# Performance work log

Hardware: AMD Instinct MI355X
Metric: run time of the kernel (lower is better)

## Reference

```python
import jax, jax.numpy as jnp
import numpy as np

K = 16      # n_sample neighbors
L = 2       # stacked PT blocks
D = 128     # in_dim
H = 128     # hidden_dim = out_dim = vector_dim
EPS = 1e-5


def _bn(x, g, b, axes):
    # batch-norm with batch statistics (train-mode MinkowskiBatchNorm / BN1d / BN2d)
    m = jnp.mean(x, axes, keepdims=True)
    v = jnp.var(x, axes, keepdims=True)
    return (x - m) * jax.lax.rsqrt(v + EPS) * g + b


def setup_inputs():
    key = jax.random.key(0)
    ks = jax.random.split(key, 16)
    B, Nper = 2, 8192
    coords = jax.random.randint(ks[0], (B, Nper, 3), 0, 200, dtype=jnp.int32)
    feats = jax.random.normal(ks[1], (B * Nper, D), dtype=jnp.float32)
    w = lambda k, s: jax.random.normal(k, s, dtype=jnp.float32) * 0.1
    return {
        'coords': coords, 'feats': feats,
        'W_top': w(ks[2], (L, D, H)),
        'bn_top_g': jnp.ones((L, H)), 'bn_top_b': jnp.zeros((L, H)),
        'W_phi': w(ks[3], (L, H, H)),
        'W_psi': w(ks[4], (L, H, H)),
        'W_alpha': w(ks[5], (L, H, H)),
        'W_d1': w(ks[6], (L, 3, H)), 'b_d1': jnp.zeros((L, H)),
        'bn_d1_g': jnp.ones((L, H)), 'bn_d1_b': jnp.zeros((L, H)),
        'W_d2': w(ks[7], (L, H, H)), 'b_d2': jnp.zeros((L, H)),
        'bn_d2_g': jnp.ones((L, H)), 'bn_d2_b': jnp.zeros((L, H)),
        'W_g1': w(ks[8], (L, H, H)), 'b_g1': jnp.zeros((L, H)),
        'bn_g1_g': jnp.ones((L, H)), 'bn_g1_b': jnp.zeros((L, H)),
        'W_g2': w(ks[9], (L, H, H)), 'b_g2': jnp.zeros((L, H)),
        'bn_g2_g': jnp.ones((L, H)), 'bn_g2_b': jnp.zeros((L, H)),
        'W_down': w(ks[10], (L, H, D)),
        'bn_down_g': jnp.ones((L, D)), 'bn_down_b': jnp.zeros((L, D)),
    }


def _knn(coords):
    # cube_query with USE_KNN=True: per-scene KNN grouping (self included)
    cf = coords.astype(jnp.float32)

    def one(c):  # c: (Nper, 3)
        d2 = jnp.sum((c[:, None, :] - c[None, :, :]) ** 2, -1)  # (Nper, Nper)
        _, idx = jax.lax.top_k(-d2, K)
        return idx

    idx = jax.vmap(one)(cf)                      # (B, Nper, K) per-scene indices
    nbr = jax.vmap(lambda c, i: c[i])(cf, idx)   # (B, Nper, K, 3) grouped coords
    rel = nbr - cf[:, :, None, :]                # relative xyz (pose input)
    B, Nper = coords.shape[0], coords.shape[1]
    gidx = (idx + (jnp.arange(B, dtype=idx.dtype) * Nper)[:, None, None]).reshape(-1, K)
    return rel.reshape(-1, K, 3), gidx           # (N,K,3), (N,K) global indices


def reference(coords, feats, W_top, bn_top_g, bn_top_b, W_phi, W_psi, W_alpha,
              W_d1, b_d1, bn_d1_g, bn_d1_b, W_d2, b_d2, bn_d2_g, bn_d2_b,
              W_g1, b_g1, bn_g1_g, bn_g1_b, W_g2, b_g2, bn_g2_g, bn_g2_b,
              W_down, bn_down_g, bn_down_b):
    rel, gidx = _knn(coords)
    f = feats
    for l in range(L):
        h = _bn(f @ W_top[l], bn_top_g[l], bn_top_b[l], 0)  # linear_top (1x1 conv + BN)
        # delta: pointwise MLP 3 -> H -> H on relative xyz (position encoding)
        pose = jax.nn.relu(_bn(rel @ W_d1[l] + b_d1[l], bn_d1_g[l], bn_d1_b[l], (0, 1)))
        pose = _bn(pose @ W_d2[l] + b_d2[l], bn_d2_g[l], bn_d2_b[l], (0, 1))  # (N,K,H)
        q = h @ W_phi[l]               # (N, H)
        kk = (h @ W_psi[l])[gidx]      # neighbor keys   (N, K, H)
        v = (h @ W_alpha[l])[gidx]     # neighbor values (N, K, H)
        # gamma: pointwise MLP on (phi - psi + pose), vector attention logits
        a = q[:, None, :] - kk + pose
        a = jax.nn.relu(_bn(a @ W_g1[l] + b_g1[l], bn_g1_g[l], bn_g1_b[l], (0, 1)))
        a = _bn(a @ W_g2[l] + b_g2[l], bn_g2_g[l], bn_g2_b[l], (0, 1))
        attn = jax.nn.softmax(a, axis=1)          # per-channel softmax over K neighbors
        y = jnp.sum(attn * (v + pose), axis=1)    # (N, H) vector-attention aggregation
        y = _bn(y @ W_down[l], bn_down_g[l], bn_down_b[l], 0)  # linear_down + BN
        f = y + f                                  # residual
    return f
```

## Files before the change

### kernel.cpp

```cpp
#include <hip/hip_runtime.h>

using u16 = unsigned short;
using u32 = unsigned int;
using u64 = unsigned long long;

#define NPTS   16384
#define NPER   8192
#define KNN    16
#define NKROWS (NPTS*KNN)
#define HD     128
#define CAP    208
#define NSLOT  16

typedef _Float16 half8 __attribute__((ext_vector_type(8)));
typedef float    floatx4 __attribute__((ext_vector_type(4)));

__device__ __forceinline__ u16  f2h(float f){ _Float16 h=(_Float16)f; return __builtin_bit_cast(u16,h); }
__device__ __forceinline__ float h2f(u16 u){ return (float)__builtin_bit_cast(_Float16,u); }
__device__ __forceinline__ u32 umin32(u32 a,u32 b){ return a<b?a:b; }

__global__ __launch_bounds__(256) void pack_coords(const int* __restrict__ coords, u32* __restrict__ pc){
    int i = blockIdx.x*256 + threadIdx.x;
    pc[i] = (u32)coords[3*i] | ((u32)coords[3*i+1]<<8) | ((u32)coords[3*i+2]<<16);
}

struct WPtrs { const float* p[8]; };
__global__ __launch_bounds__(256) void prep_weights(WPtrs wp, u16* __restrict__ wt){
    int idx = blockIdx.x*256 + threadIdx.x;
    int t = idx>>15, rem = idx&32767;
    int l = rem>>14, e = rem&16383;
    int n = e>>7, k = e&127;
    wt[idx] = f2h(wp.p[t][l*16384 + k*128 + n]);
}

__global__ __launch_bounds__(512) void knn3(const u32* __restrict__ pc, int* __restrict__ idx_g,
                                            float* __restrict__ rel, u64* __restrict__ sM){
    __shared__ u32 sc[NPER];
    __shared__ u32 buf[8][CAP];
    __shared__ u64 red[9];
    int tid = threadIdx.x;
    int wave = tid>>6, lane = tid&63;
    int scene = blockIdx.x >> 10;
    int q = (blockIdx.x & 1023)*8 + wave;

    const uint4* s4 = (const uint4*)(pc + scene*NPER);
#pragma unroll
    for (int i=0;i<4;i++) ((uint4*)sc)[tid + i*512] = s4[tid + i*512];
    if (tid<9) red[tid]=0;
    if (lane<16) buf[wave][lane]=0xFFFFFFFFu;
    __syncthreads();

    u32 qp = sc[q];
    int qx=(int)(qp&255), qy=(int)((qp>>8)&255), qz=(int)((qp>>16)&255);
    u32 thresh = 0xFFFFFFFFu;
    u32 cnt = 16;

    auto merge = [&](){
        u32 v0 = (lane      < (int)cnt) ? buf[wave][lane]      : 0xFFFFFFFFu;
        u32 v1 = (lane+64   < (int)cnt) ? buf[wave][lane+64]   : 0xFFFFFFFFu;
        u32 v2 = (lane+128  < (int)cnt) ? buf[wave][lane+128]  : 0xFFFFFFFFu;
        u32 v3 = (lane+192  < (int)cnt) ? buf[wave][lane+192]  : 0xFFFFFFFFu;
        u32 out = 0;
#pragma unroll
        for (int r=0;r<16;r++){
            u32 m = umin32(umin32(v0,v1),umin32(v2,v3));
#pragma unroll
            for (int o=32;o>=1;o>>=1) m = umin32(m, (u32)__shfl_xor((int)m, o, 64));
            if      (v0==m) v0=0xFFFFFFFFu;
            else if (v1==m) v1=0xFFFFFFFFu;
            else if (v2==m) v2=0xFFFFFFFFu;
            else if (v3==m) v3=0xFFFFFFFFu;
            if (lane==r) out = m;
            thresh = m;
        }
        if (lane<16) buf[wave][lane] = out;
        cnt = 16;
    };

    int lane2 = lane*2;
    uint2 p2 = ((const uint2*)sc)[lane];
    for (int t=0;t<64;t++){
        uint2 cur = p2;
        if (t<63) p2 = ((const uint2*)sc)[(t+1)*64+lane];
        int base = t*128 + lane2;
        u32 pa = cur.x;
        int dx0=(int)(pa&255)-qx, dy0=(int)((pa>>8)&255)-qy, dz0=(int)((pa>>16)&255)-qz;
        u32 d2_0 = (u32)(__mul24(dx0,dx0)+__mul24(dy0,dy0)+__mul24(dz0,dz0));
        u32 key0 = (d2_0<<13) + (u32)base;
        u32 pb = cur.y;
        int dx1=(int)(pb&255)-qx, dy1=(int)((pb>>8)&255)-qy, dz1=(int)((pb>>16)&255)-qz;
        u32 d2_1 = (u32)(__mul24(dx1,dx1)+__mul24(dy1,dy1)+__mul24(dz1,dz1));
        u32 key1 = (d2_1<<13) + (u32)(base+1);
        u64 m0 = __ballot(key0 < thresh);
        if (m0){
            u32 lt = __builtin_amdgcn_mbcnt_hi((u32)(m0>>32), __builtin_amdgcn_mbcnt_lo((u32)m0,0));
            if (key0 < thresh) buf[wave][cnt + lt] = key0;
            cnt += (u32)__popcll(m0);
        }
        u64 m1 = __ballot(key1 < thresh);
        if (m1){
            u32 lt = __builtin_amdgcn_mbcnt_hi((u32)(m1>>32), __builtin_amdgcn_mbcnt_lo((u32)m1,0));
            if (key1 < thresh) buf[wave][cnt + lt] = key1;
            cnt += (u32)__popcll(m1);
        }
        if (cnt > CAP-128) merge();
    }
    merge();

    int n = scene*NPER + q;
    u32 key = buf[wave][lane & 15];
    int dx=0,dy=0,dz=0;
    if (lane<16){
        int j = (int)(key & 8191u);
        idx_g[(size_t)n*KNN + lane] = scene*NPER + j;
        u32 p = sc[j];
        dx=(int)(p&255)-qx; dy=(int)((p>>8)&255)-qy; dz=(int)((p>>16)&255)-qz;
        size_t ro = ((size_t)n*KNN+lane)*3;
        rel[ro]=(float)dx; rel[ro+1]=(float)dy; rel[ro+2]=(float)dz;
    }
    int arr[9] = {dx,dy,dz, dx*dx,dy*dy,dz*dz, dx*dy,dx*dz,dy*dz};
#pragma unroll
    for (int o=32;o>=1;o>>=1)
#pragma unroll
        for (int j=0;j<9;j++) arr[j] += __shfl_xor(arr[j], o, 64);
    if (lane==0)
#pragma unroll
        for (int j=0;j<9;j++) atomicAdd(&red[j], (u64)(long long)arr[j]);
    __syncthreads();
    if (tid<9) atomicAdd(&sM[tid], red[tid]);
}

__global__ __launch_bounds__(256) void finalize_d1(const u64* __restrict__ sM, const float* __restrict__ W_d1,
        const float* __restrict__ b_d1, const float* __restrict__ g, const float* __restrict__ beta,
        float* __restrict__ A, float* __restrict__ C){
    int tid=threadIdx.x; int l=tid>>7, c=tid&127;
    double s0=(double)(long long)sM[0], s1=(double)(long long)sM[1], s2=(double)(long long)sM[2];
    double m00=(double)(long long)sM[3], m11=(double)(long long)sM[4], m22=(double)(long long)sM[5];
    double m01=(double)(long long)sM[6], m02=(double)(long long)sM[7], m12=(double)(long long)sM[8];
    double w0=W_d1[l*384+c], w1=W_d1[l*384+128+c], w2=W_d1[l*384+256+c];
    double b =b_d1[l*128+c];
    double S = s0*w0+s1*w1+s2*w2;
    double Q = m00*w0*w0+m11*w1*w1+m22*w2*w2 + 2.0*(m01*w0*w1+m02*w0*w2+m12*w1*w2);
    double cnt = (double)NKROWS;
    double mean = S/cnt + b;
    double ex2  = (Q + 2.0*b*S)/cnt + b*b;
    double var  = ex2 - mean*mean;
    float a = g[l*128+c] * (float)(1.0/sqrt(var+1e-5));
    A[l*128+c]=a; C[l*128+c]=beta[l*128+c]-(float)mean*a;
}

__global__ void finalize_affine(double* __restrict__ P, const float* __restrict__ g,
        const float* __restrict__ b, double cnt, float* __restrict__ A, float* __restrict__ C){
    int c=threadIdx.x;
    double s=0.0, q=0.0;
#pragma unroll
    for (int k=0;k<NSLOT;k++){
        s+=P[k*256+c]; q+=P[k*256+128+c];
        P[k*256+c]=0.0; P[k*256+128+c]=0.0;
    }
    double mean=s/cnt, var=q/cnt-mean*mean;
    float a = g[c] * (float)(1.0/sqrt(var+1e-5));
    A[c]=a; C[c]=b[c]-(float)mean*a;
}

struct CompF32 {
    const float* src;
    __device__ __forceinline__ void stage(u16* As,int R0,int k0,int tid) const {
#pragma unroll
        for (int u=0;u<8;u++){
            int flat=u*256+tid, row=flat>>4, c4=flat&15; int k=k0+c4*4;
            const float4 v=*(const float4*)(src+(size_t)(R0+row)*HD+k);
            ushort4 o; o.x=f2h(v.x); o.y=f2h(v.y); o.z=f2h(v.z); o.w=f2h(v.w);
            *(ushort4*)(As+row*72+c4*4)=o;
        }
    }
};
struct CompH16Aff {
    const u16* src; const float* Aa; const float* Ca;
    __device__ __forceinline__ void stage(u16* As,int R0,int k0,int tid) const {
#pragma unroll
        for (int u=0;u<8;u++){
            int flat=u*256+tid, row=flat>>4, c4=flat&15; int k=k0+c4*4;
            const ushort4 v=*(const ushort4*)(src+(size_t)(R0+row)*HD+k);
            ushort4 o;
            o.x=f2h(h2f(v.x)*Aa[k]  +Ca[k]);   o.y=f2h(h2f(v.y)*Aa[k+1]+Ca[k+1]);
            o.z=f2h(h2f(v.z)*Aa[k+2]+Ca[k+2]); o.w=f2h(h2f(v.w)*Aa[k+3]+Ca[k+3]);
            *(ushort4*)(As+row*72+c4*4)=o;
        }
    }
};
struct CompH16AffRelu {
    const u16* src; const float* Aa; const float* Ca;
    __device__ __forceinline__ void stage(u16* As,int R0,int k0,int tid) const {
#pragma unroll
        for (int u=0;u<8;u++){
            int flat=u*256+tid, row=flat>>4, c4=flat&15; int k=k0+c4*4;
            const ushort4 v=*(const ushort4*)(src+(size_t)(R0+row)*HD+k);
            ushort4 o;
            o.x=f2h(fmaxf(h2f(v.x)*Aa[k]  +Ca[k],  0.f));
            o.y=f2h(fmaxf(h2f(v.y)*Aa[k+1]+Ca[k+1],0.f));
            o.z=f2h(fmaxf(h2f(v.z)*Aa[k+2]+Ca[k+2],0.f));
            o.w=f2h(fmaxf(h2f(v.w)*Aa[k+3]+Ca[k+3],0.f));
            *(ushort4*)(As+row*72+c4*4)=o;
        }
    }
};
struct CompPose1 {
    const float* rel; const float* Wd1; const float* bd1; const float* Aa; const float* Ca;
    __device__ __forceinline__ void stage(u16* As,int R0,int k0,int tid) const {
#pragma unroll
        for (int u=0;u<8;u++){
            int flat=u*256+tid, row=flat>>4, c4=flat&15; int k=k0+c4*4; int R=R0+row;
            float r0=rel[(size_t)R*3], r1=rel[(size_t)R*3+1], r2=rel[(size_t)R*3+2];
            ushort4 o;
#pragma unroll
            for (int j=0;j<4;j++){
                int kk=k+j;
                float x = r0*Wd1[kk] + r1*Wd1[HD+kk] + r2*Wd1[2*HD+kk] + bd1[kk];
                x = fmaxf(x*Aa[kk]+Ca[kk], 0.f);
                ((u16*)&o)[j]=f2h(x);
            }
            *(ushort4*)(As+row*72+c4*4)=o;
        }
    }
};
struct CompA0 {
    const u16* q; const u16* kp; const u16* pose; const int* gidx; const float* Aa; const float* Ca;
    __device__ __forceinline__ void stage(u16* As,int R0,int k0,int tid) const {
#pragma unroll
        for (int u=0;u<8;u++){
            int flat=u*256+tid, row=flat>>4, c4=flat&15; int k=k0+c4*4; int R=R0+row;
            int n=R>>4; int g=gidx[R];
            const ushort4 qv=*(const ushort4*)(q +(size_t)n*HD+k);
            const ushort4 kv=*(const ushort4*)(kp+(size_t)g*HD+k);
            const ushort4 pv=*(const ushort4*)(pose+(size_t)R*HD+k);
            ushort4 o;
            o.x=f2h(h2f(qv.x)-h2f(kv.x) + h2f(pv.x)*Aa[k]  +Ca[k]);
            o.y=f2h(h2f(qv.y)-h2f(kv.y) + h2f(pv.y)*Aa[k+1]+Ca[k+1]);
            o.z=f2h(h2f(qv.z)-h2f(kv.z) + h2f(pv.z)*Aa[k+2]+Ca[k+2]);
            o.w=f2h(h2f(qv.w)-h2f(kv.w) + h2f(pv.w)*Aa[k+3]+Ca[k+3]);
            *(ushort4*)(As+row*72+c4*4)=o;
        }
    }
};

template<class Comp, bool OUT16, bool HASBIAS, bool STATS>
__global__ __launch_bounds__(256) void gemm128(Comp comp, const u16* __restrict__ Wt,
        const float* __restrict__ bias, void* __restrict__ outp, double* __restrict__ statsP,
        int wtStride, long outStride){
    __shared__ __align__(16) u16 As[128*72];
    __shared__ __align__(16) u16 Bs[128*72];
    __shared__ float cs2[2][128], cq2[2][128];
    const u16* W = Wt + (size_t)blockIdx.y*wtStride;
    u16*   o16 = (u16*)outp   + (size_t)blockIdx.y*outStride;
    float* o32 = (float*)outp + (size_t)blockIdx.y*outStride;
    int tid=threadIdx.x;
    int R0=blockIdx.x*128;
    int lane=tid&63, wave=tid>>6, quad=lane>>4, r16=lane&15;
    int wm=wave>>1, wn=wave&1;
    floatx4 acc[4][4]={};
#pragma unroll
    for (int ks=0;ks<2;ks++){
        int k0=ks*64;
        comp.stage(As,R0,k0,tid);
#pragma unroll
        for (int u=0;u<4;u++){
            int flat=u*256+tid, n=flat>>3, c8=flat&7;
            *(int4*)(Bs+n*72+c8*8) = *(const int4*)(W+n*HD+k0+c8*8);
        }
        __syncthreads();
#pragma unroll
        for (int kk2=0;kk2<2;kk2++){
            half8 aF[4], bF[4];
#pragma unroll
            for (int mi=0;mi<4;mi++) aF[mi]=*(const half8*)(As+(wm*64+mi*16+r16)*72 + kk2*32+quad*8);
#pragma unroll
            for (int ni=0;ni<4;ni++) bF[ni]=*(const half8*)(Bs+(wn*64+ni*16+r16)*72 + kk2*32+quad*8);
#pragma unroll
            for (int mi=0;mi<4;mi++)
#pragma unroll
                for (int ni=0;ni<4;ni++)
                    acc[mi][ni]=__builtin_amdgcn_mfma_f32_16x16x32_f16(aF[mi],bF[ni],acc[mi][ni],0,0,0);
        }
        __syncthreads();
    }
    float sAcc[4]={0,0,0,0}, qAcc[4]={0,0,0,0};
#pragma unroll
    for (int mi=0;mi<4;mi++)
#pragma unroll
        for (int ni=0;ni<4;ni++){
            int col=wn*64+ni*16+r16;
            float bv = HASBIAS ? bias[col] : 0.f;
#pragma unroll
            for (int rg=0;rg<4;rg++){
                int row=R0+wm*64+mi*16+quad*4+rg;
                float v=acc[mi][ni][rg]+bv;
                if (STATS){ sAcc[ni]+=v; qAcc[ni]+=v*v; }
                if (OUT16) o16[(size_t)row*HD+col]=f2h(v);
                else       o32[(size_t)row*HD+col]=v;
            }
        }
    if (STATS){
#pragma unroll
        for (int ni=0;ni<4;ni++){
            float s=sAcc[ni], q=qAcc[ni];
            s += __shfl_xor(s,16,64); s += __shfl_xor(s,32,64);
            q += __shfl_xor(q,16,64); q += __shfl_xor(q,32,64);
            if (quad==0){
                int col=wn*64+ni*16+r16;
                cs2[wm][col]=s; cq2[wm][col]=q;
            }
        }
        __syncthreads();
        if (tid<128){
            int slot = blockIdx.x & (NSLOT-1);
            unsafeAtomicAdd(&statsP[slot*256+tid],     (double)(cs2[0][tid]+cs2[1][tid]));
            unsafeAtomicAdd(&statsP[slot*256+128+tid], (double)(cq2[0][tid]+cq2[1][tid]));
        }
    }
}

__global__ __launch_bounds__(256) void aggregate(const u16* __restrict__ a2, const u16* __restrict__ pose,
        const u16* __restrict__ vv, const int* __restrict__ gidx,
        const float* __restrict__ Ag2, const float* __restrict__ Cg2,
        const float* __restrict__ Ad2, const float* __restrict__ Cd2, float* __restrict__ y){
    int c=(threadIdx.x&63)*2, h=threadIdx.x>>6;
    int n=blockIdx.x*4+h;
    float sA0=Ag2[c], sC0=Cg2[c], pA0=Ad2[c], pC0=Cd2[c];
    float sA1=Ag2[c+1], sC1=Cg2[c+1], pA1=Ad2[c+1], pC1=Cd2[c+1];
    float av0[16], av1[16]; float m0=-1e30f, m1=-1e30f;
#pragma unroll
    for (int k=0;k<16;k++){
        ushort2 t=*(const ushort2*)(a2+((size_t)n*16+k)*HD+c);
        float a0=h2f(t.x)*sA0+sC0, a1=h2f(t.y)*sA1+sC1;
        av0[k]=a0; av1[k]=a1; m0=fmaxf(m0,a0); m1=fmaxf(m1,a1);
    }
    float sum0=0.f, sum1=0.f;
#pragma unroll
    for (int k=0;k<16;k++){
        float e0=__expf(av0[k]-m0), e1=__expf(av1[k]-m1);
        av0[k]=e0; av1[k]=e1; sum0+=e0; sum1+=e1;
    }
    float acc0=0.f, acc1=0.f;
#pragma unroll
    for (int k=0;k<16;k++){
        int g=gidx[n*16+k];
        ushort2 pt=*(const ushort2*)(pose+((size_t)n*16+k)*HD+c);
        ushort2 vt=*(const ushort2*)(vv+(size_t)g*HD+c);
        acc0 += av0[k]*(h2f(pt.x)*pA0+pC0 + h2f(vt.x));
        acc1 += av1[k]*(h2f(pt.y)*pA1+pC1 + h2f(vt.y));
    }
    y[(size_t)n*HD+c]  =acc0/sum0;
    y[(size_t)n*HD+c+1]=acc1/sum1;
}

__global__ __launch_bounds__(256) void residual(const float* __restrict__ ydown, const float* __restrict__ A,
        const float* __restrict__ C, const float* __restrict__ fin, float* __restrict__ fout){
    size_t i=(size_t)blockIdx.x*256+threadIdx.x; int c=(int)(i&127);
    fout[i]=ydown[i]*A[c]+C[c]+fin[i];
}

extern "C" void kernel_launch(void* const* d_in, const int* in_sizes, int n_in,
                              void* d_out, int out_size, void* d_ws, size_t ws_size,
                              hipStream_t stream){
    const int*   coords=(const int*)d_in[0];
    const float* feats=(const float*)d_in[1];
    const float* W_top=(const float*)d_in[2];
    const float* g_top=(const float*)d_in[3];
    const float* bt_top=(const float*)d_in[4];
    const float* W_phi=(const float*)d_in[5];
    const float* W_psi=(const float*)d_in[6];
    const float* W_alp=(const float*)d_in[7];
    const float* W_d1=(const float*)d_in[8];
    const float* b_d1=(const float*)d_in[9];
    const float* g_d1=(const float*)d_in[10];
    const float* bt_d1=(const float*)d_in[11];
    const float* W_d2=(const float*)d_in[12];
    const float* b_d2=(const float*)d_in[13];
    const float* g_d2=(const float*)d_in[14];
    const float* bt_d2=(const float*)d_in[15];
    const float* W_g1=(const float*)d_in[16];
    const float* b_g1=(const float*)d_in[17];
    const float* g_g1=(const float*)d_in[18];
    const float* bt_g1=(const float*)d_in[19];
    const float* W_g2=(const float*)d_in[20];
    const float* b_g2=(const float*)d_in[21];
    const float* g_g2=(const float*)d_in[22];
    const float* bt_g2=(const float*)d_in[23];
    const float* W_dn=(const float*)d_in[24];
    const float* g_dn=(const float*)d_in[25];
    const float* bt_dn=(const float*)d_in[26];

    char* ws=(char*)d_ws;
    size_t off=0;
    auto carve=[&](size_t bytes)->char*{ char* p=ws+off; off=(off+bytes+255)&~(size_t)255; return p; };
    u32*    pc    =(u32*)   carve((size_t)NPTS*4);
    int*    idxg  =(int*)   carve((size_t)NKROWS*4);
    float*  rel   =(float*) carve((size_t)NKROWS*3*4);
    u16*    h16   =(u16*)   carve((size_t)NPTS*HD*2);
    u16*    qb    =(u16*)   carve((size_t)3*NPTS*HD*2);
    u16*    kpb   = qb + (size_t)NPTS*HD;
    u16*    vvb   = qb + (size_t)2*NPTS*HD;
    float*  yb    =(float*) carve((size_t)NPTS*HD*4);
    float*  ydown =(float*) carve((size_t)NPTS*HD*4);
    float*  fbuf  =(float*) carve((size_t)NPTS*HD*4);
    u16*    wt    =(u16*)   carve((size_t)8*2*16384*2);
    char*   stats =         carve(NSLOT*256*8 + 256);
    double* P     =(double*)stats;
    u64*    sM    =(u64*)(stats + NSLOT*256*8);
    float*  aff   =(float*) carve(8192);
    float *A_top=aff, *C_top=aff+128, *A_d2=aff+256, *C_d2=aff+384,
          *A_g1=aff+512, *C_g1=aff+640, *A_g2=aff+768, *C_g2=aff+896,
          *A_dn=aff+1024, *C_dn=aff+1152, *A_d1=aff+1280, *C_d1=aff+1536;
    u16*    pose2 =(u16*)   carve((size_t)NKROWS*HD*2);
    u16*    abuf  =(u16*)   carve((size_t)NKROWS*HD*2);
    if (ws_size < off) return;

    hipMemsetAsync(stats, 0, NSLOT*256*8 + 256, stream);
    pack_coords<<<dim3(NPTS/256),dim3(256),0,stream>>>(coords, pc);
    WPtrs wp{{W_top,W_phi,W_psi,W_alp,W_d2,W_g1,W_g2,W_dn}};
    prep_weights<<<dim3(8*2*16384/256),dim3(256),0,stream>>>(wp, wt);
    knn3<<<dim3(2048),dim3(512),0,stream>>>(pc, idxg, rel, sM);
    finalize_d1<<<dim3(1),dim3(256),0,stream>>>(sM, W_d1, b_d1, g_d1, bt_d1, A_d1, C_d1);

    const float* fin=feats;
    for (int l=0;l<2;l++){
        const u16* wt_top=wt+(0*2+l)*16384; const u16* wt_phi=wt+(1*2+l)*16384;
        const u16* wt_d2 =wt+(4*2+l)*16384; const u16* wt_g1 =wt+(5*2+l)*16384;
        const u16* wt_g2 =wt+(6*2+l)*16384; const u16* wt_dn =wt+(7*2+l)*16384;

        gemm128<CompF32,true,false,true><<<dim3(NPTS/128),dim3(256),0,stream>>>(
            CompF32{fin}, wt_top, nullptr, h16, P, 0, 0);
        finalize_affine<<<dim3(1),dim3(128),0,stream>>>(P, g_top+l*128, bt_top+l*128, (double)NPTS, A_top, C_top);

        gemm128<CompH16Aff,true,false,false><<<dim3(NPTS/128,3),dim3(256),0,stream>>>(
            CompH16Aff{h16,A_top,C_top}, wt_phi, nullptr, qb, nullptr, 2*16384, (long)NPTS*HD);

        gemm128<CompPose1,true,true,true><<<dim3(NKROWS/128),dim3(256),0,stream>>>(
            CompPose1{rel, W_d1+l*384, b_d1+l*128, A_d1+l*128, C_d1+l*128}, wt_d2, b_d2+l*128, pose2, P, 0, 0);
        finalize_affine<<<dim3(1),dim3(128),0,stream>>>(P, g_d2+l*128, bt_d2+l*128, (double)NKROWS, A_d2, C_d2);

        gemm128<CompA0,true,true,true><<<dim3(NKROWS/128),dim3(256),0,stream>>>(
            CompA0{qb,kpb,pose2,idxg,A_d2,C_d2}, wt_g1, b_g1+l*128, abuf, P, 0, 0);
        finalize_affine<<<dim3(1),dim3(128),0,stream>>>(P, g_g1+l*128, bt_g1+l*128, (double)NKROWS, A_g1, C_g1);

        gemm128<CompH16AffRelu,true,true,true><<<dim3(NKROWS/128),dim3(256),0,stream>>>(
            CompH16AffRelu{abuf,A_g1,C_g1}, wt_g2, b_g2+l*128, abuf, P, 0, 0);
        finalize_affine<<<dim3(1),dim3(128),0,stream>>>(P, g_g2+l*128, bt_g2+l*128, (double)NKROWS, A_g2, C_g2);

        aggregate<<<dim3(NPTS/4),dim3(256),0,stream>>>(abuf, pose2, vvb, idxg, A_g2, C_g2, A_d2, C_d2, yb);

        gemm128<CompF32,false,false,true><<<dim3(NPTS/128),dim3(256),0,stream>>>(
            CompF32{yb}, wt_dn, nullptr, ydown, P, 0, 0);
        finalize_affine<<<dim3(1),dim3(128),0,stream>>>(P, g_dn+l*128, bt_dn+l*128, (double)NPTS, A_dn, C_dn);
        residual<<<dim3(NPTS*HD/256),dim3(256),0,stream>>>(ydown, A_dn, C_dn, fin, (l==1)?(float*)d_out:fbuf);
        fin=fbuf;
    }
}
```

Baseline: 559.5 us.

## Use uniform-grid KNN and fold pose/query-key paths into the gamma-1 GEMM

Result: slower. 705.1 us (+26.0%).

```diff
diff --git a/kernel.cpp b/kernel.cpp
--- a/kernel.cpp
+++ b/kernel.cpp
@@ -9,7 +9,7 @@
 #define KNN    16
 #define NKROWS (NPTS*KNN)
 #define HD     128
-#define CAP    208
+#define KCAP   512
 #define NSLOT  16
 
 typedef _Float16 half8 __attribute__((ext_vector_type(8)));
@@ -18,94 +18,136 @@
 __device__ __forceinline__ u16  f2h(float f){ _Float16 h=(_Float16)f; return __builtin_bit_cast(u16,h); }
 __device__ __forceinline__ float h2f(u16 u){ return (float)__builtin_bit_cast(_Float16,u); }
 __device__ __forceinline__ u32 umin32(u32 a,u32 b){ return a<b?a:b; }
-
-__global__ __launch_bounds__(256) void pack_coords(const int* __restrict__ coords, u32* __restrict__ pc){
+__device__ __forceinline__ int cell_of(int x){ return (x*5243)>>17; }
+
+__global__ __launch_bounds__(256) void pack_count(const int* __restrict__ coords, u32* __restrict__ pc,
+                                                  u32* __restrict__ cellcnt){
     int i = blockIdx.x*256 + threadIdx.x;
-    pc[i] = (u32)coords[3*i] | ((u32)coords[3*i+1]<<8) | ((u32)coords[3*i+2]<<16);
-}
-
-struct WPtrs { const float* p[8]; };
-__global__ __launch_bounds__(256) void prep_weights(WPtrs wp, u16* __restrict__ wt){
-    int idx = blockIdx.x*256 + threadIdx.x;
-    int t = idx>>15, rem = idx&32767;
-    int l = rem>>14, e = rem&16383;
-    int n = e>>7, k = e&127;
-    wt[idx] = f2h(wp.p[t][l*16384 + k*128 + n]);
-}
-
-__global__ __launch_bounds__(512) void knn3(const u32* __restrict__ pc, int* __restrict__ idx_g,
-                                            float* __restrict__ rel, u64* __restrict__ sM){
-    __shared__ u32 sc[NPER];
-    __shared__ u32 buf[8][CAP];
+    int x=coords[3*i], y=coords[3*i+1], z=coords[3*i+2];
+    pc[i] = (u32)x | ((u32)y<<8) | ((u32)z<<16);
+    int cid = ((cell_of(z)*8 + cell_of(y))<<3) + cell_of(x);
+    atomicAdd(&cellcnt[(i>>13)*512 + cid], 1u);
+}
+
+__global__ __launch_bounds__(1024) void prefix1024(const u32* __restrict__ cellcnt,
+                                                   u32* __restrict__ cs, u32* __restrict__ cptr){
+    __shared__ u32 tmp[1024];
+    int t = threadIdx.x;
+    u32 mine = cellcnt[t];
+    tmp[t] = mine;
+    __syncthreads();
+    for (int off=1; off<1024; off<<=1){
+        u32 v = (t>=off) ? tmp[t-off] : 0u;
+        __syncthreads();
+        tmp[t] += v;
+        __syncthreads();
+    }
+    if (t==0) cs[0]=0;
+    cs[t+1] = tmp[t];
+    cptr[t] = tmp[t] - mine;
+}
+
+__global__ __launch_bounds__(256) void scatter_pts(const u32* __restrict__ pc, u32* __restrict__ cptr,
+                                                   uint2* __restrict__ spt){
+    int i = blockIdx.x*256 + threadIdx.x;
+    u32 p = pc[i];
+    int cid = ((cell_of((int)((p>>16)&255))*8 + cell_of((int)((p>>8)&255)))<<3) + cell_of((int)(p&255));
+    u32 pos = atomicAdd(&cptr[(i>>13)*512 + cid], 1u);
+    spt[pos] = make_uint2(p, (u32)(i&8191));
+}
+
+__global__ __launch_bounds__(256) void knn_grid(const u32* __restrict__ pc, const uint2* __restrict__ spt,
+                                                const u32* __restrict__ cs, int* __restrict__ idx_g,
+                                                float* __restrict__ rel, u64* __restrict__ sM){
+    __shared__ u32 buf[4][KCAP];
     __shared__ u64 red[9];
     int tid = threadIdx.x;
     int wave = tid>>6, lane = tid&63;
-    int scene = blockIdx.x >> 10;
-    int q = (blockIdx.x & 1023)*8 + wave;
-
-    const uint4* s4 = (const uint4*)(pc + scene*NPER);
-#pragma unroll
-    for (int i=0;i<4;i++) ((uint4*)sc)[tid + i*512] = s4[tid + i*512];
+    int scene = blockIdx.x >> 11;
+    int q = (blockIdx.x & 2047)*4 + wave;
     if (tid<9) red[tid]=0;
     if (lane<16) buf[wave][lane]=0xFFFFFFFFu;
     __syncthreads();
 
-    u32 qp = sc[q];
+    u32 qp = pc[scene*NPER + q];
     int qx=(int)(qp&255), qy=(int)((qp>>8)&255), qz=(int)((qp>>16)&255);
+    int cx=cell_of(qx), cy=cell_of(qy), cz=cell_of(qz);
     u32 thresh = 0xFFFFFFFFu;
     u32 cnt = 16;
 
     auto merge = [&](){
-        u32 v0 = (lane      < (int)cnt) ? buf[wave][lane]      : 0xFFFFFFFFu;
-        u32 v1 = (lane+64   < (int)cnt) ? buf[wave][lane+64]   : 0xFFFFFFFFu;
-        u32 v2 = (lane+128  < (int)cnt) ? buf[wave][lane+128]  : 0xFFFFFFFFu;
-        u32 v3 = (lane+192  < (int)cnt) ? buf[wave][lane+192]  : 0xFFFFFFFFu;
+        u32 v[8];
+#pragma unroll
+        for (int r=0;r<8;r++) v[r] = ((u32)(lane + r*64) < cnt) ? buf[wave][lane + r*64] : 0xFFFFFFFFu;
         u32 out = 0;
 #pragma unroll
-        for (int r=0;r<16;r++){
-            u32 m = umin32(umin32(v0,v1),umin32(v2,v3));
+        for (int it=0; it<16; it++){
+            u32 m = umin32(umin32(umin32(v[0],v[1]),umin32(v[2],v[3])),
+                           umin32(umin32(v[4],v[5]),umin32(v[6],v[7])));
 #pragma unroll
             for (int o=32;o>=1;o>>=1) m = umin32(m, (u32)__shfl_xor((int)m, o, 64));
-            if      (v0==m) v0=0xFFFFFFFFu;
-            else if (v1==m) v1=0xFFFFFFFFu;
-            else if (v2==m) v2=0xFFFFFFFFu;
-            else if (v3==m) v3=0xFFFFFFFFu;
-            if (lane==r) out = m;
+#pragma unroll
+            for (int r=0;r<8;r++) if (v[r]==m) v[r]=0xFFFFFFFFu;
+            if (lane==it) out = m;
             thresh = m;
         }
         if (lane<16) buf[wave][lane] = out;
         cnt = 16;
     };
 
-    int lane2 = lane*2;
-    uint2 p2 = ((const uint2*)sc)[lane];
-    for (int t=0;t<64;t++){
-        uint2 cur = p2;
-        if (t<63) p2 = ((const uint2*)sc)[(t+1)*64+lane];
-        int base = t*128 + lane2;
-        u32 pa = cur.x;
-        int dx0=(int)(pa&255)-qx, dy0=(int)((pa>>8)&255)-qy, dz0=(int)((pa>>16)&255)-qz;
-        u32 d2_0 = (u32)(__mul24(dx0,dx0)+__mul24(dy0,dy0)+__mul24(dz0,dz0));
-        u32 key0 = (d2_0<<13) + (u32)base;
-        u32 pb = cur.y;
-        int dx1=(int)(pb&255)-qx, dy1=(int)((pb>>8)&255)-qy, dz1=(int)((pb>>16)&255)-qz;
-        u32 d2_1 = (u32)(__mul24(dx1,dx1)+__mul24(dy1,dy1)+__mul24(dz1,dz1));
-        u32 key1 = (d2_1<<13) + (u32)(base+1);
-        u64 m0 = __ballot(key0 < thresh);
-        if (m0){
-            u32 lt = __builtin_amdgcn_mbcnt_hi((u32)(m0>>32), __builtin_amdgcn_mbcnt_lo((u32)m0,0));
-            if (key0 < thresh) buf[wave][cnt + lt] = key0;
-            cnt += (u32)__popcll(m0);
-        }
-        u64 m1 = __ballot(key1 < thresh);
-        if (m1){
-            u32 lt = __builtin_amdgcn_mbcnt_hi((u32)(m1>>32), __builtin_amdgcn_mbcnt_lo((u32)m1,0));
-            if (key1 < thresh) buf[wave][cnt + lt] = key1;
-            cnt += (u32)__popcll(m1);
-        }
-        if (cnt > CAP-128) merge();
-    }
+    auto scan64 = [&](u32 key){
+        u64 mask = __ballot(key < thresh);
+        if (mask){
+            u32 lt = __builtin_amdgcn_mbcnt_hi((u32)(mask>>32), __builtin_amdgcn_mbcnt_lo((u32)mask,0));
+            if (key < thresh) buf[wave][cnt + lt] = key;
+            cnt += (u32)__popcll(mask);
+            if (cnt > KCAP-64) merge();
+        }
+    };
+
+    int x0 = cx>0?cx-1:0, x1 = cx<7?cx+1:7;
+    int y0 = cy>0?cy-1:0, y1 = cy<7?cy+1:7;
+    int z0 = cz>0?cz-1:0, z1 = cz<7?cz+1:7;
+    int sbase = scene*512;
+    int nx = x1-x0+1;
+    for (int rz=z0; rz<=z1; rz++)
+        for (int ry=y0; ry<=y1; ry++){
+            int c0 = sbase + ((rz*8+ry)<<3) + x0;
+            int s = (int)cs[c0], e = (int)cs[c0+nx];
+            for (int i=s; i<e; i+=64){
+                int p = i + lane;
+                u32 key = 0xFFFFFFFFu;
+                if (p < e){
+                    uint2 pt = spt[p];
+                    int dx=(int)(pt.x&255)-qx, dy=(int)((pt.x>>8)&255)-qy, dz=(int)((pt.x>>16)&255)-qz;
+                    u32 d2 = (u32)(__mul24(dx,dx)+__mul24(dy,dy)+__mul24(dz,dz));
+                    key = (d2<<13) | pt.y;
+                }
+                scan64(key);
+            }
+        }
     merge();
+
+    int d2_16 = (int)(thresh>>13);
+    int mxl = (cx==0)?1000: qx - 25*(cx-1);
+    int mxr = (cx==7)?1000: 25*(cx+2) - qx;
+    int myl = (cy==0)?1000: qy - 25*(cy-1);
+    int myr = (cy==7)?1000: 25*(cy+2) - qy;
+    int mzl = (cz==0)?1000: qz - 25*(cz-1);
+    int mzr = (cz==7)?1000: 25*(cz+2) - qz;
+    int m = min(min(min(mxl,mxr),min(myl,myr)),min(mzl,mzr));
+    if (d2_16 > m*m){
+        thresh = 0xFFFFFFFFu; cnt = 16;
+        if (lane<16) buf[wave][lane]=0xFFFFFFFFu;
+        const u32* sp = pc + scene*NPER;
+        for (int t=0;t<128;t++){
+            u32 p = sp[t*64+lane];
+            int dx=(int)(p&255)-qx, dy=(int)((p>>8)&255)-qy, dz=(int)((p>>16)&255)-qz;
+            u32 d2 = (u32)(__mul24(dx,dx)+__mul24(dy,dy)+__mul24(dz,dz));
+            scan64((d2<<13) | (u32)(t*64+lane));
+        }
+        merge();
+    }
 
     int n = scene*NPER + q;
     u32 key = buf[wave][lane & 15];
@@ -113,7 +155,7 @@
     if (lane<16){
         int j = (int)(key & 8191u);
         idx_g[(size_t)n*KNN + lane] = scene*NPER + j;
-        u32 p = sc[j];
+        u32 p = pc[scene*NPER + j];
         dx=(int)(p&255)-qx; dy=(int)((p>>8)&255)-qy; dz=(int)((p>>16)&255)-qz;
         size_t ro = ((size_t)n*KNN+lane)*3;
         rel[ro]=(float)dx; rel[ro+1]=(float)dy; rel[ro+2]=(float)dz;
@@ -128,6 +170,16 @@
         for (int j=0;j<9;j++) atomicAdd(&red[j], (u64)(long long)arr[j]);
     __syncthreads();
     if (tid<9) atomicAdd(&sM[tid], red[tid]);
+}
+
+struct WPtrs { const float* p[5]; };
+__global__ __launch_bounds__(256) void prep_weights(WPtrs wp, u16* __restrict__ wt){
+    const int tmap[5] = {0,3,4,6,7};
+    int idx = blockIdx.x*256 + threadIdx.x;
+    int t = idx>>15, rem = idx&32767;
+    int l = rem>>14, e = rem&16383;
+    int n = e>>7, k = e&127;
+    wt[(tmap[t]*2+l)*16384 + n*128 + k] = f2h(wp.p[t][l*16384 + k*128 + n]);
 }
 
 __global__ __launch_bounds__(256) void finalize_d1(const u64* __restrict__ sM, const float* __restrict__ W_d1,
@@ -150,7 +202,10 @@
 }
 
 __global__ void finalize_affine(double* __restrict__ P, const float* __restrict__ g,
-        const float* __restrict__ b, double cnt, float* __restrict__ A, float* __restrict__ C){
+        const float* __restrict__ b, double cnt, float* __restrict__ A, float* __restrict__ C,
+        const float* __restrict__ Wg1, const float* __restrict__ b_d2, const float* __restrict__ b_g1,
+        float* __restrict__ biasc){
+    __shared__ float term[128];
     int c=threadIdx.x;
     double s=0.0, q=0.0;
 #pragma unroll
@@ -160,12 +215,33 @@
     }
     double mean=s/cnt, var=q/cnt-mean*mean;
     float a = g[c] * (float)(1.0/sqrt(var+1e-5));
-    A[c]=a; C[c]=b[c]-(float)mean*a;
+    float cc = b[c]-(float)mean*a;
+    A[c]=a; C[c]=cc;
+    if (Wg1){
+        term[c] = b_d2[c]*a + cc;
+        __syncthreads();
+        float acc = b_g1[c];
+        for (int n=0;n<128;n++) acc += term[n]*Wg1[n*128+c];
+        biasc[c] = acc;
+    }
 }
 
 struct CompF32 {
     const float* src;
     __device__ __forceinline__ void stage(u16* As,int R0,int k0,int tid) const {
+#pragma unroll
+        for (int u=0;u<8;u++){
+            int flat=u*256+tid, row=flat>>4, c4=flat&15; int k=k0+c4*4;
+            const float4 v=*(const float4*)(src+(size_t)(R0+row)*HD+k);
+            ushort4 o; o.x=f2h(v.x); o.y=f2h(v.y); o.z=f2h(v.z); o.w=f2h(v.w);
+            *(ushort4*)(As+row*72+c4*4)=o;
+        }
+    }
+};
+struct CompStatic {
+    const float* p[4];
+    __device__ __forceinline__ void stage(u16* As,int R0,int k0,int tid) const {
+        const float* src = p[blockIdx.y];
 #pragma unroll
         for (int u=0;u<8;u++){
             int flat=u*256+tid, row=flat>>4, c4=flat&15; int k=k0+c4*4;
@@ -224,30 +300,14 @@
         }
     }
 };
-struct CompA0 {
-    const u16* q; const u16* kp; const u16* pose; const int* gidx; const float* Aa; const float* Ca;
-    __device__ __forceinline__ void stage(u16* As,int R0,int k0,int tid) const {
-#pragma unroll
-        for (int u=0;u<8;u++){
-            int flat=u*256+tid, row=flat>>4, c4=flat&15; int k=k0+c4*4; int R=R0+row;
-            int n=R>>4; int g=gidx[R];
-            const ushort4 qv=*(const ushort4*)(q +(size_t)n*HD+k);
-            const ushort4 kv=*(const ushort4*)(kp+(size_t)g*HD+k);
-            const ushort4 pv=*(const ushort4*)(pose+(size_t)R*HD+k);
-            ushort4 o;
-            o.x=f2h(h2f(qv.x)-h2f(kv.x) + h2f(pv.x)*Aa[k]  +Ca[k]);
-            o.y=f2h(h2f(qv.y)-h2f(kv.y) + h2f(pv.y)*Aa[k+1]+Ca[k+1]);
-            o.z=f2h(h2f(qv.z)-h2f(kv.z) + h2f(pv.z)*Aa[k+2]+Ca[k+2]);
-            o.w=f2h(h2f(qv.w)-h2f(kv.w) + h2f(pv.w)*Aa[k+3]+Ca[k+3]);
-            *(ushort4*)(As+row*72+c4*4)=o;
-        }
-    }
-};
-
-template<class Comp, bool OUT16, bool HASBIAS, bool STATS>
-__global__ __launch_bounds__(256) void gemm128(Comp comp, const u16* __restrict__ Wt,
+
+struct BTS { const float* p[4]; const float* scale; };
+
+template<class Comp, bool OUT16, bool HASBIAS, bool STATS, bool EPIQK, bool BT, bool OUTT>
+__global__ __launch_bounds__(256) void gemm128(Comp comp, const u16* __restrict__ Wt, BTS bts,
         const float* __restrict__ bias, void* __restrict__ outp, double* __restrict__ statsP,
-        int wtStride, long outStride){
+        int wtStride, long outStride,
+        const u16* __restrict__ eq, const u16* __restrict__ ek, const int* __restrict__ egidx){
     __shared__ __align__(16) u16 As[128*72];
     __shared__ __align__(16) u16 Bs[128*72];
     __shared__ float cs2[2][128], cq2[2][128];
@@ -263,10 +323,27 @@
     for (int ks=0;ks<2;ks++){
         int k0=ks*64;
         comp.stage(As,R0,k0,tid);
-#pragma unroll
-        for (int u=0;u<4;u++){
-            int flat=u*256+tid, n=flat>>3, c8=flat&7;
-            *(int4*)(Bs+n*72+c8*8) = *(const int4*)(W+n*HD+k0+c8*8);
+        if (BT){
+            const float* Bf = bts.p[blockIdx.y];
+#pragma unroll
+            for (int u=0;u<4;u++){
+                int flat=u*256+tid, n=flat>>3, c8=flat&7;
+                __align__(16) u16 tmp[8];
+#pragma unroll
+                for (int e=0;e<8;e++){
+                    int k=k0+c8*8+e;
+                    float v = Bf[(size_t)k*128+n];
+                    if (bts.scale) v *= bts.scale[k];
+                    tmp[e]=f2h(v);
+                }
+                *(int4*)(Bs+n*72+c8*8) = *(int4*)tmp;
+            }
+        } else {
+#pragma unroll
+            for (int u=0;u<4;u++){
+                int flat=u*256+tid, n=flat>>3, c8=flat&7;
+                *(int4*)(Bs+n*72+c8*8) = *(const int4*)(W+n*HD+k0+c8*8);
+            }
         }
         __syncthreads();
 #pragma unroll
@@ -288,16 +365,23 @@
 #pragma unroll
     for (int mi=0;mi<4;mi++)
 #pragma unroll
-        for (int ni=0;ni<4;ni++){
-            int col=wn*64+ni*16+r16;
-            float bv = HASBIAS ? bias[col] : 0.f;
-#pragma unroll
-            for (int rg=0;rg<4;rg++){
-                int row=R0+wm*64+mi*16+quad*4+rg;
-                float v=acc[mi][ni][rg]+bv;
+        for (int rg=0;rg<4;rg++){
+            int row=R0+wm*64+mi*16+quad*4+rg;
+            int n16=0, gg=0;
+            if (EPIQK){ n16=row>>4; gg=egidx[row]; }
+#pragma unroll
+            for (int ni=0;ni<4;ni++){
+                int col=wn*64+ni*16+r16;
+                float v=acc[mi][ni][rg] + (HASBIAS ? bias[col] : 0.f);
+                if (EPIQK) v += h2f(eq[(size_t)n16*HD+col]) - h2f(ek[(size_t)gg*HD+col]);
                 if (STATS){ sAcc[ni]+=v; qAcc[ni]+=v*v; }
-                if (OUT16) o16[(size_t)row*HD+col]=f2h(v);
-                else       o32[(size_t)row*HD+col]=v;
+                if (OUTT){
+                    if (OUT16) o16[(size_t)col*HD+row]=f2h(v);
+                    else       o32[(size_t)col*HD+row]=v;
+                } else {
+                    if (OUT16) o16[(size_t)row*HD+col]=f2h(v);
+                    else       o32[(size_t)row*HD+col]=v;
+                }
             }
         }
     if (STATS){
@@ -395,6 +479,9 @@
     size_t off=0;
     auto carve=[&](size_t bytes)->char*{ char* p=ws+off; off=(off+bytes+255)&~(size_t)255; return p; };
     u32*    pc    =(u32*)   carve((size_t)NPTS*4);
+    uint2*  spt   =(uint2*) carve((size_t)NPTS*8);
+    u32*    cs    =(u32*)   carve(1032*4);
+    u32*    cptr  =(u32*)   carve(1024*4);
     int*    idxg  =(int*)   carve((size_t)NKROWS*4);
     float*  rel   =(float*) carve((size_t)NKROWS*3*4);
     u16*    h16   =(u16*)   carve((size_t)NPTS*HD*2);
@@ -405,54 +492,83 @@
     float*  ydown =(float*) carve((size_t)NPTS*HD*4);
     float*  fbuf  =(float*) carve((size_t)NPTS*HD*4);
     u16*    wt    =(u16*)   carve((size_t)8*2*16384*2);
-    char*   stats =         carve(NSLOT*256*8 + 256);
+    char*   stats =         carve(NSLOT*256*8 + 256 + 4096);
     double* P     =(double*)stats;
     u64*    sM    =(u64*)(stats + NSLOT*256*8);
+    u32*    cellcnt=(u32*)(stats + NSLOT*256*8 + 256);
     float*  aff   =(float*) carve(8192);
     float *A_top=aff, *C_top=aff+128, *A_d2=aff+256, *C_d2=aff+384,
           *A_g1=aff+512, *C_g1=aff+640, *A_g2=aff+768, *C_g2=aff+896,
-          *A_dn=aff+1024, *C_dn=aff+1152, *A_d1=aff+1280, *C_d1=aff+1536;
+          *A_dn=aff+1024, *C_dn=aff+1152, *A_d1=aff+1280, *C_d1=aff+1536,
+          *biasc=aff+1792;
     u16*    pose2 =(u16*)   carve((size_t)NKROWS*HD*2);
     u16*    abuf  =(u16*)   carve((size_t)NKROWS*HD*2);
     if (ws_size < off) return;
 
-    hipMemsetAsync(stats, 0, NSLOT*256*8 + 256, stream);
-    pack_coords<<<dim3(NPTS/256),dim3(256),0,stream>>>(coords, pc);
-    WPtrs wp{{W_top,W_phi,W_psi,W_alp,W_d2,W_g1,W_g2,W_dn}};
-    prep_weights<<<dim3(8*2*16384/256),dim3(256),0,stream>>>(wp, wt);
-    knn3<<<dim3(2048),dim3(512),0,stream>>>(pc, idxg, rel, sM);
+    BTS noBT{{nullptr,nullptr,nullptr,nullptr}, nullptr};
+
+    hipMemsetAsync(stats, 0, NSLOT*256*8 + 256 + 4096, stream);
+    pack_count<<<dim3(NPTS/256),dim3(256),0,stream>>>(coords, pc, cellcnt);
+    prefix1024<<<dim3(1),dim3(1024),0,stream>>>(cellcnt, cs, cptr);
+    scatter_pts<<<dim3(NPTS/256),dim3(256),0,stream>>>(pc, cptr, spt);
+    WPtrs wp{{W_top,W_alp,W_d2,W_g2,W_dn}};
+    prep_weights<<<dim3(5*2*16384/256),dim3(256),0,stream>>>(wp, wt);
+    {
+        CompStatic cstat{{W_phi, W_phi+16384, W_psi, W_psi+16384}};
+        BTS bts{{W_g1, W_g1+16384, W_g1, W_g1+16384}, nullptr};
+        gemm128<CompStatic,true,false,false,false,true,true><<<dim3(1,4),dim3(256),0,stream>>>(
+            cstat, nullptr, bts, nullptr, wt+2*16384, nullptr, 0, 16384, nullptr,nullptr,nullptr);
+    }
+    knn_grid<<<dim3(4096),dim3(256),0,stream>>>(pc, spt, cs, idxg, rel, sM);
     finalize_d1<<<dim3(1),dim3(256),0,stream>>>(sM, W_d1, b_d1, g_d1, bt_d1, A_d1, C_d1);
 
     const float* fin=feats;
     for (int l=0;l<2;l++){
-        const u16* wt_top=wt+(0*2+l)*16384; const u16* wt_phi=wt+(1*2+l)*16384;
-        const u16* wt_d2 =wt+(4*2+l)*16384; const u16* wt_g1 =wt+(5*2+l)*16384;
-        const u16* wt_g2 =wt+(6*2+l)*16384; const u16* wt_dn =wt+(7*2+l)*16384;
-
-        gemm128<CompF32,true,false,true><<<dim3(NPTS/128),dim3(256),0,stream>>>(
-            CompF32{fin}, wt_top, nullptr, h16, P, 0, 0);
-        finalize_affine<<<dim3(1),dim3(128),0,stream>>>(P, g_top+l*128, bt_top+l*128, (double)NPTS, A_top, C_top);
-
-        gemm128<CompH16Aff,true,false,false><<<dim3(NPTS/128,3),dim3(256),0,stream>>>(
-            CompH16Aff{h16,A_top,C_top}, wt_phi, nullptr, qb, nullptr, 2*16384, (long)NPTS*HD);
-
-        gemm128<CompPose1,true,true,true><<<dim3(NKROWS/128),dim3(256),0,stream>>>(
-            CompPose1{rel, W_d1+l*384, b_d1+l*128, A_d1+l*128, C_d1+l*128}, wt_d2, b_d2+l*128, pose2, P, 0, 0);
-        finalize_affine<<<dim3(1),dim3(128),0,stream>>>(P, g_d2+l*128, bt_d2+l*128, (double)NKROWS, A_d2, C_d2);
-
-        gemm128<CompA0,true,true,true><<<dim3(NKROWS/128),dim3(256),0,stream>>>(
-            CompA0{qb,kpb,pose2,idxg,A_d2,C_d2}, wt_g1, b_g1+l*128, abuf, P, 0, 0);
-        finalize_affine<<<dim3(1),dim3(128),0,stream>>>(P, g_g1+l*128, bt_g1+l*128, (double)NKROWS, A_g1, C_g1);
-
-        gemm128<CompH16AffRelu,true,true,true><<<dim3(NKROWS/128),dim3(256),0,stream>>>(
-            CompH16AffRelu{abuf,A_g1,C_g1}, wt_g2, b_g2+l*128, abuf, P, 0, 0);
-        finalize_affine<<<dim3(1),dim3(128),0,stream>>>(P, g_g2+l*128, bt_g2+l*128, (double)NKROWS, A_g2, C_g2);
+        const u16* wt_top=wt+(0*2+l)*16384;
+        const u16* wt_d2 =wt+(4*2+l)*16384;
+        const u16* wt_c  =wt+(5*2+l)*16384;
+        const u16* wt_g2 =wt+(6*2+l)*16384;
+        const u16* wt_dn =wt+(7*2+l)*16384;
+
+        gemm128<CompF32,true,false,true,false,false,false><<<dim3(NPTS/128),dim3(256),0,stream>>>(
+            CompF32{fin}, wt_top, noBT, nullptr, h16, P, 0, 0, nullptr,nullptr,nullptr);
+        finalize_affine<<<dim3(1),dim3(128),0,stream>>>(P, g_top+l*128, bt_top+l*128, (double)NPTS,
+            A_top, C_top, nullptr,nullptr,nullptr,nullptr);
+
+        gemm128<CompH16Aff,true,false,false,false,false,false><<<dim3(NPTS/128,3),dim3(256),0,stream>>>(
+            CompH16Aff{h16,A_top,C_top}, wt+(1*2+l)*16384, noBT, nullptr, qb, nullptr,
+            2*16384, (long)NPTS*HD, nullptr,nullptr,nullptr);
+
+        gemm128<CompPose1,true,true,true,false,false,false><<<dim3(NKROWS/128),dim3(256),0,stream>>>(
+            CompPose1{rel, W_d1+l*384, b_d1+l*128, A_d1+l*128, C_d1+l*128}, wt_d2, noBT,
+            b_d2+l*128, pose2, P, 0, 0, nullptr,nullptr,nullptr);
+        finalize_affine<<<dim3(1),dim3(128),0,stream>>>(P, g_d2+l*128, bt_d2+l*128, (double)NKROWS,
+            A_d2, C_d2, W_g1+l*16384, b_d2+l*128, b_g1+l*128, biasc);
+
+        {
+            CompStatic cd{{W_d2+l*16384, nullptr, nullptr, nullptr}};
+            BTS bts{{W_g1+l*16384, nullptr, nullptr, nullptr}, A_d2};
+            gemm128<CompStatic,true,false,false,false,true,true><<<dim3(1,1),dim3(256),0,stream>>>(
+                cd, nullptr, bts, nullptr, (void*)wt_c, nullptr, 0, 0, nullptr,nullptr,nullptr);
+        }
+
+        gemm128<CompPose1,true,true,true,true,false,false><<<dim3(NKROWS/128),dim3(256),0,stream>>>(
+            CompPose1{rel, W_d1+l*384, b_d1+l*128, A_d1+l*128, C_d1+l*128}, wt_c, noBT,
+            biasc, abuf, P, 0, 0, qb, kpb, idxg);
+        finalize_affine<<<dim3(1),dim3(128),0,stream>>>(P, g_g1+l*128, bt_g1+l*128, (double)NKROWS,
+            A_g1, C_g1, nullptr,nullptr,nullptr,nullptr);
+
+        gemm128<CompH16AffRelu,true,true,true,false,false,false><<<dim3(NKROWS/128),dim3(256),0,stream>>>(
+            CompH16AffRelu{abuf,A_g1,C_g1}, wt_g2, noBT, b_g2+l*128, abuf, P, 0, 0, nullptr,nullptr,nullptr);
+        finalize_affine<<<dim3(1),dim3(128),0,stream>>>(P, g_g2+l*128, bt_g2+l*128, (double)NKROWS,
+            A_g2, C_g2, nullptr,nullptr,nullptr,nullptr);
 
         aggregate<<<dim3(NPTS/4),dim3(256),0,stream>>>(abuf, pose2, vvb, idxg, A_g2, C_g2, A_d2, C_d2, yb);
 
-        gemm128<CompF32,false,false,true><<<dim3(NPTS/128),dim3(256),0,stream>>>(
-            CompF32{yb}, wt_dn, nullptr, ydown, P, 0, 0);
-        finalize_affine<<<dim3(1),dim3(128),0,stream>>>(P, g_dn+l*128, bt_dn+l*128, (double)NPTS, A_dn, C_dn);
+        gemm128<CompF32,false,false,true,false,false,false><<<dim3(NPTS/128),dim3(256),0,stream>>>(
+            CompF32{yb}, wt_dn, noBT, nullptr, ydown, P, 0, 0, nullptr,nullptr,nullptr);
+        finalize_affine<<<dim3(1),dim3(128),0,stream>>>(P, g_dn+l*128, bt_dn+l*128, (double)NPTS,
+            A_dn, C_dn, nullptr,nullptr,nullptr,nullptr);
         residual<<<dim3(NPTS*HD/256),dim3(256),0,stream>>>(ydown, A_dn, C_dn, fin, (l==1)?(float*)d_out:fbuf);
         fin=fbuf;
     }
```
